# Kernel tuning notes

Hardware: AMD Instinct MI355X
Metric: run time of the kernel (lower is better)

Reference implementation:

```python
import jax, jax.numpy as jnp
import numpy as np

DIM = 768
NUM_HEADS = 12
HEAD_DIM = DIM // NUM_HEADS
H, W = 16, 64
HK, WK = 7, 11
N = H * W
B = 8
SCALE = HEAD_DIM ** -0.5


def build_local_mask():
    # Vectorized version of the original nested loop: for each token (h,w),
    # positions inside the hk x wk window are visible (0), others -inf.
    h_idx = np.repeat(np.arange(H), W)  # [N]
    w_idx = np.tile(np.arange(W), H)    # [N]
    hh = np.arange(H + HK - 1)
    ww = np.arange(W + WK - 1)
    in_h = (hh[None, :] >= h_idx[:, None]) & (hh[None, :] < h_idx[:, None] + HK)  # [N, H+hk-1]
    in_w = (ww[None, :] >= w_idx[:, None]) & (ww[None, :] < w_idx[:, None] + WK)  # [N, W+wk-1]
    visible = in_h[:, :, None] & in_w[:, None, :]  # [N, H+hk-1, W+wk-1]
    mask_big = np.where(visible, 0.0, 1.0).astype(np.float32)
    mask_crop = mask_big[:, HK // 2:H + HK // 2, WK // 2:W + WK // 2].reshape(N, N)
    mask = np.where(mask_crop < 1.0, mask_crop, np.float32(-np.inf))  # [N, N]
    return jnp.asarray(mask)[None, None]  # [1, 1, N, N]


def setup_inputs() -> dict:
    key = jax.random.key(0)
    k1, k2, k3 = jax.random.split(key, 3)
    x = jax.random.normal(k1, (B, N, DIM), dtype=jnp.float32)
    w_qkv = jax.random.normal(k2, (3 * DIM, DIM), dtype=jnp.float32) * 0.02  # torch Linear weight [out,in]
    w_proj = jax.random.normal(k3, (DIM, DIM), dtype=jnp.float32) * 0.02
    b_proj = jnp.zeros((DIM,), dtype=jnp.float32)
    mask = build_local_mask()
    return {"x": x, "w_qkv": w_qkv, "w_proj": w_proj, "b_proj": b_proj, "mask": mask}


def reference(x, w_qkv, w_proj, b_proj, mask):
    Bx, Nx, C = x.shape
    qkv = jnp.einsum('bnc,oc->bno', x, w_qkv)  # [B, N, 3*dim]
    qkv = qkv.reshape(Bx, Nx, 3, NUM_HEADS, HEAD_DIM).transpose(2, 0, 3, 1, 4)  # [3,B,h,N,d]
    q, k, v = qkv[0] * SCALE, qkv[1], qkv[2]
    attn = jnp.einsum('bhnd,bhmd->bhnm', q, k) + mask  # [B,h,N,N] with local -inf mask
    attn = jax.nn.softmax(attn, axis=-1)
    out = jnp.einsum('bhnm,bhmd->bhnd', attn, v)  # [B,h,N,d]
    out = out.transpose(0, 2, 1, 3).reshape(Bx, Nx, C)
    out = jnp.einsum('bnc,oc->bno', out, w_proj) + b_proj
    return out
```

## Files before the change

### kernel.cpp

```cpp
#include <hip/hip_runtime.h>
#include <hip/hip_bf16.h>
#include <stdint.h>

typedef __bf16 bf16;
typedef __bf16 bf16x8 __attribute__((ext_vector_type(8)));
typedef __bf16 bf16x4 __attribute__((ext_vector_type(4)));
typedef float f32x4 __attribute__((ext_vector_type(4)));

#define KDIM 768
#define NHEAD 12
#define HDIM 64
#define NTOK 1024
#define BATCH 8

#define SWZ(row, b) ((b) ^ (((row) & 7) << 4))

__device__ __forceinline__ void gl_lds16(const bf16* g, bf16* l) {
    __builtin_amdgcn_global_load_lds((const __attribute__((address_space(1))) void*)g,
                                     (__attribute__((address_space(3))) void*)l, 16, 0, 0);
}

#define G_MFMA(a, b, c) __builtin_amdgcn_mfma_f32_16x16x32_bf16(a, b, c, 0, 0, 0)
#define VMW(N) asm volatile("s_waitcnt vmcnt(" #N ")" ::: "memory")

__global__ void k_cvt_all(const float* __restrict__ x, const float* __restrict__ wq,
                          const float* __restrict__ wp, bf16* __restrict__ xb,
                          bf16* __restrict__ wqb, bf16* __restrict__ wpb) {
    int b = blockIdx.x;
    const float* src;
    bf16* dst;
    int base;
    if (b < 6144)       { src = x;  dst = xb;  base = b; }
    else if (b < 7872)  { src = wq; dst = wqb; base = b - 6144; }
    else                { src = wp; dst = wpb; base = b - 7872; }
    int i = (base * 256 + threadIdx.x) * 4;
    float4 v = *(const float4*)(src + i);
    bf16x4 o;
    o[0] = (bf16)v.x; o[1] = (bf16)v.y; o[2] = (bf16)v.z; o[3] = (bf16)v.w;
    *(bf16x4*)(dst + i) = o;
}

#define QTILE(S, kA, kB, doA, doB, vmn) do {                                    \
    const char* A8 = (const char*)sA[S];                                        \
    const char* B8 = (const char*)sB[S];                                        \
    bf16x8 af[2], bfr[6];                                                       \
    af[0] = *(const bf16x8*)(A8 + (wr * 64 + 0 + lr) * 64 + kxoff);             \
    af[1] = *(const bf16x8*)(A8 + (wr * 64 + 16 + lr) * 64 + kxoff);            \
    _Pragma("unroll")                                                           \
    for (int n = 0; n < 6; ++n)                                                 \
        bfr[n] = *(const bf16x8*)(B8 + (wc * 96 + n * 16 + lr) * 64 + kxoff);   \
    if (doA) {                                                                  \
        const bf16* p_ = Ast + (size_t)(kA) * 32;                               \
        gl_lds16(p_,                    &sA[(S) ^ 1][t * 8]);                   \
        gl_lds16(p_ + (size_t)64 * KDIM, &sA[(S) ^ 1][t * 8 + 2048]);           \
    }                                                                           \
    __builtin_amdgcn_s_setprio(1);                                              \
    _Pragma("unroll")                                                           \
    for (int m = 0; m < 2; ++m)                                                 \
        _Pragma("unroll")                                                       \
        for (int n = 0; n < 6; ++n)                                             \
            acc[m][n] = G_MFMA(af[m], bfr[n], acc[m][n]);                       \
    __builtin_amdgcn_s_setprio(0);                                              \
    __builtin_amdgcn_s_barrier();                                               \
    af[0] = *(const bf16x8*)(A8 + (wr * 64 + 32 + lr) * 64 + kxoff);            \
    af[1] = *(const bf16x8*)(A8 + (wr * 64 + 48 + lr) * 64 + kxoff);            \
    if (doB) {                                                                  \
        const bf16* p_ = Wst + (size_t)(kB) * 32;                               \
        gl_lds16(p_,                     &sB[S][t * 8]);                        \
        gl_lds16(p_ + (size_t)64 * KDIM,  &sB[S][t * 8 + 2048]);                \
        gl_lds16(p_ + (size_t)128 * KDIM, &sB[S][t * 8 + 4096]);                \
    }                                                                           \
    __builtin_amdgcn_s_setprio(1);                                              \
    _Pragma("unroll")                                                           \
    for (int m = 0; m < 2; ++m)                                                 \
        _Pragma("unroll")                                                       \
        for (int n = 0; n < 6; ++n)                                             \
            acc[m + 2][n] = G_MFMA(af[m], bfr[n], acc[m + 2][n]);               \
    __builtin_amdgcn_s_setprio(0);                                              \
    if ((vmn) == 3) { VMW(3); } else if ((vmn) == 0) { VMW(0); }                \
    __builtin_amdgcn_s_barrier();                                               \
} while (0)

#define GEMM192_PRE(A_PTR, W_PTR)                                               \
    const int t = threadIdx.x;                                                  \
    const int lane = t & 63;                                                    \
    const int wv = t >> 6;                                                      \
    const int wr = wv >> 1, wc = wv & 1;                                        \
    const int lr = lane & 15, lg = lane >> 4;                                   \
    const int kxoff = (lg << 4) ^ (((lr >> 1) & 3) << 4);                       \
    const int srow = t >> 2;                                                    \
    const int spos = ((t & 3) ^ ((t >> 3) & 3)) * 8;                            \
    const int bm = blockIdx.x, bn = blockIdx.y;                                 \
    const bf16* Ab = (A_PTR) + (size_t)bm * 128 * KDIM;                         \
    const bf16* Wb = (W_PTR) + (size_t)bn * 192 * KDIM;                         \
    const bf16* Ast = Ab + (size_t)srow * KDIM + spos;                          \
    const bf16* Wst = Wb + (size_t)srow * KDIM + spos;                          \
    f32x4 acc[4][6] = {};                                                       \
    gl_lds16(Ast,                     &sA[0][t * 8]);                           \
    gl_lds16(Ast + (size_t)64 * KDIM, &sA[0][t * 8 + 2048]);                    \
    gl_lds16(Wst,                      &sB[0][t * 8]);                          \
    gl_lds16(Wst + (size_t)64 * KDIM,  &sB[0][t * 8 + 2048]);                   \
    gl_lds16(Wst + (size_t)128 * KDIM, &sB[0][t * 8 + 4096]);                   \
    gl_lds16(Wst + 32,                      &sB[1][t * 8]);                     \
    gl_lds16(Wst + 32 + (size_t)64 * KDIM,  &sB[1][t * 8 + 2048]);              \
    gl_lds16(Wst + 32 + (size_t)128 * KDIM, &sB[1][t * 8 + 4096]);              \
    VMW(3);                                                                     \
    __builtin_amdgcn_s_barrier();                                               \
    _Pragma("unroll 1")                                                         \
    for (int g = 0; g < 11; ++g) {                                              \
        QTILE(0, 2 * g + 1, 2 * g + 2, 1, 1, 3);                                \
        QTILE(1, 2 * g + 2, 2 * g + 3, 1, 1, 3);                                \
    }                                                                           \
    QTILE(0, 23, 0, 1, 0, 0);                                                   \
    QTILE(1, 0, 0, 0, 0, -1);

__global__ __launch_bounds__(256, 3) void k_gemm_qkv(
    const bf16* __restrict__ A, const bf16* __restrict__ W,
    bf16* __restrict__ qb, bf16* __restrict__ kb, bf16* __restrict__ vb)
{
    __shared__ __attribute__((aligned(16))) bf16 sA[2][4096];
    __shared__ __attribute__((aligned(16))) bf16 sB[2][6144];
    GEMM192_PRE(A, W);

    const float QSC = 0.18033688011112042f;
#pragma unroll
    for (int n = 0; n < 6; ++n) {
        int o = bn * 192 + wc * 96 + n * 16 + lr;
        int s = o / 768;
        int rem = o - s * 768;
        int head = rem >> 6;
        int d = o & 63;
        bf16* dst = (s == 0) ? qb : ((s == 1) ? kb : vb);
        float sc = (s == 0) ? QSC : 1.0f;
#pragma unroll
        for (int m = 0; m < 4; ++m) {
            int grow = bm * 128 + wr * 64 + m * 16 + lg * 4;
            int bidx = grow >> 10;
            int tok = grow & 1023;
            size_t base = (((size_t)bidx * NHEAD + head) * NTOK + tok) * HDIM + d;
#pragma unroll
            for (int r = 0; r < 4; ++r)
                dst[base + (size_t)r * HDIM] = (bf16)(acc[m][n][r] * sc);
        }
    }
}

__global__ __launch_bounds__(256, 3) void k_gemm_proj(
    const bf16* __restrict__ A, const bf16* __restrict__ W,
    const float* __restrict__ bias, float* __restrict__ out)
{
    __shared__ __attribute__((aligned(16))) bf16 sA[2][4096];
    __shared__ __attribute__((aligned(16))) bf16 sB[2][6144];
    GEMM192_PRE(A, W);

#pragma unroll
    for (int n = 0; n < 6; ++n) {
        int col = bn * 192 + wc * 96 + n * 16 + lr;
        float bv = bias[col];
#pragma unroll
        for (int m = 0; m < 4; ++m) {
            int grow = bm * 128 + wr * 64 + m * 16 + lg * 4;
#pragma unroll
            for (int r = 0; r < 4; ++r)
                out[(size_t)(grow + r) * KDIM + col] = acc[m][n][r] + bv;
        }
    }
}

__global__ __launch_bounds__(256) void k_attn(
    const bf16* __restrict__ qbuf, const bf16* __restrict__ kbuf,
    const bf16* __restrict__ vbuf, bf16* __restrict__ ob)
{
    const int x = blockIdx.x;
    const int sub = x >> 3;
    const int bh = (x & 7) * 12 + (sub >> 4);
    const int qblk = sub & 15;
    const int head = bh % NHEAD, bidx = bh / NHEAD;
    const bf16* Q  = qbuf + (size_t)bh * NTOK * HDIM;
    const bf16* Kp = kbuf + (size_t)bh * NTOK * HDIM;
    const bf16* Vp = vbuf + (size_t)bh * NTOK * HDIM;

    const int t = threadIdx.x, lane = t & 63, wv = t >> 6;
    const int lr = lane & 15, lg = lane >> 4, lkb = lg * 8;

    __shared__ bf16 Ks[2][64 * 64];
    __shared__ bf16 vT[2][64 * 64];
    __shared__ bf16 pls[4][16 * 64];

    {
        bf16x8 z = {};
        *(bf16x8*)&pls[wv][lane * 16] = z;
        *(bf16x8*)&pls[wv][lane * 16 + 8] = z;
    }

    bf16x8 qf[2];
#pragma unroll
    for (int ks = 0; ks < 2; ++ks)
        qf[ks] = *(const bf16x8*)(Q + (size_t)(qblk * 64 + wv * 16 + lr) * HDIM + ks * 32 + lkb);

    f32x4 acc[4] = {};
    float lrow[4] = {0.f, 0.f, 0.f, 0.f};

    const int kh0 = (qblk - 3 < 0) ? 0 : qblk - 3;
    const int kh1 = (qblk + 3 > 15) ? 15 : qblk + 3;

    const int sj = t >> 2;
    const int sd = (t & 3) * 16;

    const bf16* ks0 = Kp + (size_t)(kh0 * 64 + sj) * HDIM + sd;
    const bf16* vs0 = Vp + (size_t)(kh0 * 64 + sj) * HDIM + sd;
    bf16x8 gk0 = *(const bf16x8*)ks0, gk1 = *(const bf16x8*)(ks0 + 8);
    bf16x8 gv0 = *(const bf16x8*)vs0, gv1 = *(const bf16x8*)(vs0 + 8);

    char* pb8 = (char*)pls[wv];
    const int wq0 = wv * 16 + lg * 4;
    int cur = 0;

    for (int kh = kh0; kh <= kh1; ++kh) {
        char* kb8 = (char*)Ks[cur];
        char* vb8 = (char*)vT[cur];
        {
            int kbo = sj * 128 + sd * 2;
            *(bf16x8*)(kb8 + SWZ(sj, kbo)) = gk0;
            *(bf16x8*)(kb8 + SWZ(sj, kbo + 16)) = gk1;
        }
#pragma unroll
        for (int ii = 0; ii < 8; ++ii) {
            int d = sd + ii;
            *(bf16*)(vb8 + SWZ(d, (d << 7) + (sj << 1))) = gv0[ii];
        }
#pragma unroll
        for (int ii = 0; ii < 8; ++ii) {
            int d = sd + 8 + ii;
            *(bf16*)(vb8 + SWZ(d, (d << 7) + (sj << 1))) = gv1[ii];
        }
        if (kh < kh1) {
            const bf16* kn = Kp + (size_t)((kh + 1) * 64 + sj) * HDIM + sd;
            const bf16* vn = Vp + (size_t)((kh + 1) * 64 + sj) * HDIM + sd;
            gk0 = *(const bf16x8*)kn; gk1 = *(const bf16x8*)(kn + 8);
            gv0 = *(const bf16x8*)vn; gv1 = *(const bf16x8*)(vn + 8);
        }
        asm volatile("s_waitcnt lgkmcnt(0)" ::: "memory");
        __builtin_amdgcn_s_barrier();

        float psum[4] = {0.f, 0.f, 0.f, 0.f};
#pragma unroll
        for (int jj = 0; jj < 3; ++jj) {
            int j = wv - 1 + jj;
            if (j >= 0 && j <= 3) {
                int key = j * 16 + lr;
                int kbase = key * 128;
                bf16x8 kf0 = *(const bf16x8*)(kb8 + SWZ(key, kbase + lg * 16));
                bf16x8 kf1 = *(const bf16x8*)(kb8 + SWZ(key, kbase + 64 + lg * 16));
                f32x4 sv = {};
                sv = G_MFMA(qf[0], kf0, sv);
                sv = G_MFMA(qf[1], kf1, sv);
#pragma unroll
                for (int r = 0; r < 4; ++r) {
                    int dw = wq0 + r - key;
                    float p = (dw >= -5 && dw <= 5) ? exp2f(sv[r]) : 0.0f;
                    psum[r] += p;
                    int row = lg * 4 + r;
                    *(bf16*)(pb8 + SWZ(row, row * 128 + key * 2)) = (bf16)p;
                }
            }
        }
#pragma unroll
        for (int r = 0; r < 4; ++r) lrow[r] += psum[r];

        bf16x8 pf0 = *(const bf16x8*)(pb8 + SWZ(lr, lr * 128 + lg * 16));
        bf16x8 pf1 = *(const bf16x8*)(pb8 + SWZ(lr, lr * 128 + 64 + lg * 16));
#pragma unroll
        for (int dt = 0; dt < 4; ++dt) {
            int vrow = dt * 16 + lr;
            bf16x8 vf0 = *(const bf16x8*)(vb8 + SWZ(vrow, vrow * 128 + lg * 16));
            bf16x8 vf1 = *(const bf16x8*)(vb8 + SWZ(vrow, vrow * 128 + 64 + lg * 16));
            acc[dt] = G_MFMA(pf0, vf0, acc[dt]);
            acc[dt] = G_MFMA(pf1, vf1, acc[dt]);
        }
        cur ^= 1;
    }

#pragma unroll
    for (int off = 1; off < 16; off <<= 1)
#pragma unroll
        for (int r = 0; r < 4; ++r) lrow[r] += __shfl_xor(lrow[r], off);

#pragma unroll
    for (int r = 0; r < 4; ++r) {
        float inv = 1.0f / lrow[r];
        int tok = qblk * 64 + wv * 16 + lg * 4 + r;
        size_t rowbase = ((size_t)bidx * NTOK + tok) * KDIM + head * HDIM;
#pragma unroll
        for (int dt = 0; dt < 4; ++dt)
            ob[rowbase + dt * 16 + lr] = (bf16)(acc[dt][r] * inv);
    }
}

extern "C" void kernel_launch(void* const* d_in, const int* in_sizes, int n_in,
                              void* d_out, int out_size, void* d_ws, size_t ws_size,
                              hipStream_t stream) {
    const float* x      = (const float*)d_in[0];
    const float* w_qkv  = (const float*)d_in[1];
    const float* w_proj = (const float*)d_in[2];
    const float* b_proj = (const float*)d_in[3];
    float* out = (float*)d_out;

    char* ws = (char*)d_ws;
    bf16* xb  = (bf16*)(ws);
    bf16* wqb = (bf16*)(ws + 12582912);
    bf16* wpb = (bf16*)(ws + 16121856);
    bf16* qb  = (bf16*)(ws + 17301504);
    bf16* kb  = (bf16*)(ws + 29884416);
    bf16* vb  = (bf16*)(ws + 42467328);
    bf16* aob = (bf16*)(ws + 55050240);

    hipLaunchKernelGGL(k_cvt_all, dim3(8448), dim3(256), 0, stream, x, w_qkv, w_proj, xb, wqb, wpb);
    hipLaunchKernelGGL(k_gemm_qkv, dim3(64, 12), dim3(256), 0, stream, xb, wqb, qb, kb, vb);
    hipLaunchKernelGGL(k_attn,     dim3(1536), dim3(256), 0, stream, qb, kb, vb, aob);
    hipLaunchKernelGGL(k_gemm_proj, dim3(64, 4), dim3(256), 0, stream, aob, wpb, b_proj, out);
}
```

Measured before the change: 101.2 us.

## Fuse fp32-to-bf16 conversion of x into the QKV GEMM A-tile loads

The separate pass that converts x to bf16 is removed. The QKV GEMM now streams fp32 x tiles straight into LDS through global_load_lds and converts them to bf16 when it builds the MFMA fragments. This avoids writing and re-reading a 12.5 MB bf16 copy of x. In exchange the A tile takes twice the LDS and load bandwidth per k-step, occupancy drops from 3 to 2 blocks, and every fragment read now costs extra conversion ALU work.

```diff
diff --git a/kernel.cpp b/kernel.cpp
--- a/kernel.cpp
+++ b/kernel.cpp
@@ -19,25 +19,153 @@
     __builtin_amdgcn_global_load_lds((const __attribute__((address_space(1))) void*)g,
                                      (__attribute__((address_space(3))) void*)l, 16, 0, 0);
 }
+__device__ __forceinline__ void gl_lds16f(const float* g, float* l) {
+    __builtin_amdgcn_global_load_lds((const __attribute__((address_space(1))) void*)g,
+                                     (__attribute__((address_space(3))) void*)l, 16, 0, 0);
+}
 
 #define G_MFMA(a, b, c) __builtin_amdgcn_mfma_f32_16x16x32_bf16(a, b, c, 0, 0, 0)
 #define VMW(N) asm volatile("s_waitcnt vmcnt(" #N ")" ::: "memory")
 
-__global__ void k_cvt_all(const float* __restrict__ x, const float* __restrict__ wq,
-                          const float* __restrict__ wp, bf16* __restrict__ xb,
-                          bf16* __restrict__ wqb, bf16* __restrict__ wpb) {
+__global__ void k_cvt_w(const float* __restrict__ wq, const float* __restrict__ wp,
+                        bf16* __restrict__ wqb, bf16* __restrict__ wpb) {
     int b = blockIdx.x;
     const float* src;
     bf16* dst;
     int base;
-    if (b < 6144)       { src = x;  dst = xb;  base = b; }
-    else if (b < 7872)  { src = wq; dst = wqb; base = b - 6144; }
-    else                { src = wp; dst = wpb; base = b - 7872; }
+    if (b < 1728) { src = wq; dst = wqb; base = b; }
+    else          { src = wp; dst = wpb; base = b - 1728; }
     int i = (base * 256 + threadIdx.x) * 4;
     float4 v = *(const float4*)(src + i);
     bf16x4 o;
     o[0] = (bf16)v.x; o[1] = (bf16)v.y; o[2] = (bf16)v.z; o[3] = (bf16)v.w;
     *(bf16x4*)(dst + i) = o;
+}
+
+
+#define AFRAG(dst, A8, row) do {                                                \
+    const int rb_ = (row) * 128;                                                \
+    float4 w0_ = *(const float4*)((A8) + rb_ + a0off);                          \
+    float4 w1_ = *(const float4*)((A8) + rb_ + a1off);                          \
+    dst[0] = (bf16)w0_.x; dst[1] = (bf16)w0_.y;                                 \
+    dst[2] = (bf16)w0_.z; dst[3] = (bf16)w0_.w;                                 \
+    dst[4] = (bf16)w1_.x; dst[5] = (bf16)w1_.y;                                 \
+    dst[6] = (bf16)w1_.z; dst[7] = (bf16)w1_.w;                                 \
+} while (0)
+
+#define QTILEF(S, kA, kB, doA, doB, vmn) do {                                   \
+    const char* A8 = (const char*)sAf[S];                                       \
+    const char* B8 = (const char*)sB[S];                                        \
+    bf16x8 af[2], bfr[6];                                                       \
+    AFRAG(af[0], A8, wr * 64 + 0 + lr);                                         \
+    AFRAG(af[1], A8, wr * 64 + 16 + lr);                                        \
+    _Pragma("unroll")                                                           \
+    for (int n = 0; n < 6; ++n)                                                 \
+        bfr[n] = *(const bf16x8*)(B8 + (wc * 96 + n * 16 + lr) * 64 + kxoff);   \
+    if (doA) {                                                                  \
+        const float* p_ = XAst + (size_t)(kA) * 32;                             \
+        float* d_ = &sAf[(S) ^ 1][t * 4];                                       \
+        gl_lds16f(p_,                       d_);                                \
+        gl_lds16f(p_ + (size_t)32 * KDIM,   d_ + 1024);                         \
+        gl_lds16f(p_ + (size_t)64 * KDIM,   d_ + 2048);                         \
+        gl_lds16f(p_ + (size_t)96 * KDIM,   d_ + 3072);                         \
+    }                                                                           \
+    __builtin_amdgcn_s_setprio(1);                                              \
+    _Pragma("unroll")                                                           \
+    for (int m = 0; m < 2; ++m)                                                 \
+        _Pragma("unroll")                                                       \
+        for (int n = 0; n < 6; ++n)                                             \
+            acc[m][n] = G_MFMA(af[m], bfr[n], acc[m][n]);                       \
+    __builtin_amdgcn_s_setprio(0);                                              \
+    __builtin_amdgcn_s_barrier();                                               \
+    AFRAG(af[0], A8, wr * 64 + 32 + lr);                                        \
+    AFRAG(af[1], A8, wr * 64 + 48 + lr);                                        \
+    if (doB) {                                                                  \
+        const bf16* p_ = Wst + (size_t)(kB) * 32;                               \
+        gl_lds16(p_,                     &sB[S][t * 8]);                        \
+        gl_lds16(p_ + (size_t)64 * KDIM,  &sB[S][t * 8 + 2048]);                \
+        gl_lds16(p_ + (size_t)128 * KDIM, &sB[S][t * 8 + 4096]);                \
+    }                                                                           \
+    __builtin_amdgcn_s_setprio(1);                                              \
+    _Pragma("unroll")                                                           \
+    for (int m = 0; m < 2; ++m)                                                 \
+        _Pragma("unroll")                                                       \
+        for (int n = 0; n < 6; ++n)                                             \
+            acc[m + 2][n] = G_MFMA(af[m], bfr[n], acc[m + 2][n]);               \
+    __builtin_amdgcn_s_setprio(0);                                              \
+    if ((vmn) == 3) { VMW(3); } else if ((vmn) == 0) { VMW(0); }                \
+    __builtin_amdgcn_s_barrier();                                               \
+} while (0)
+
+__global__ __launch_bounds__(256, 2) void k_gemm_qkv(
+    const float* __restrict__ X, const bf16* __restrict__ W,
+    bf16* __restrict__ qb, bf16* __restrict__ kb, bf16* __restrict__ vb)
+{
+    __shared__ __attribute__((aligned(16))) float sAf[2][4096];
+    __shared__ __attribute__((aligned(16))) bf16 sB[2][6144];
+    const int t = threadIdx.x;
+    const int lane = t & 63;
+    const int wv = t >> 6;
+    const int wr = wv >> 1, wc = wv & 1;
+    const int lr = lane & 15, lg = lane >> 4;
+    const int kxoff = (lg << 4) ^ (((lr >> 1) & 3) << 4);
+    const int xorb4 = (lr & 7) << 4;
+    const int a0off = (lg << 5) ^ xorb4;
+    const int a1off = ((lg << 5) | 16) ^ xorb4;
+    const int srow = t >> 2;
+    const int spos = ((t & 3) ^ ((t >> 3) & 3)) * 8;
+    const int bm = blockIdx.x, bn = blockIdx.y;
+    const float* XAst = X + (size_t)(bm * 128 + (t >> 3)) * KDIM
+                          + (size_t)(((t & 7) ^ ((t >> 3) & 7)) * 4);
+    const bf16* Wb = W + (size_t)bn * 192 * KDIM;
+    const bf16* Wst = Wb + (size_t)srow * KDIM + spos;
+    f32x4 acc[4][6] = {};
+
+    {
+        float* d_ = &sAf[0][t * 4];
+        gl_lds16f(XAst,                       d_);
+        gl_lds16f(XAst + (size_t)32 * KDIM,   d_ + 1024);
+        gl_lds16f(XAst + (size_t)64 * KDIM,   d_ + 2048);
+        gl_lds16f(XAst + (size_t)96 * KDIM,   d_ + 3072);
+    }
+    gl_lds16(Wst,                      &sB[0][t * 8]);
+    gl_lds16(Wst + (size_t)64 * KDIM,  &sB[0][t * 8 + 2048]);
+    gl_lds16(Wst + (size_t)128 * KDIM, &sB[0][t * 8 + 4096]);
+    gl_lds16(Wst + 32,                      &sB[1][t * 8]);
+    gl_lds16(Wst + 32 + (size_t)64 * KDIM,  &sB[1][t * 8 + 2048]);
+    gl_lds16(Wst + 32 + (size_t)128 * KDIM, &sB[1][t * 8 + 4096]);
+    VMW(3);
+    __builtin_amdgcn_s_barrier();
+
+#pragma unroll 1
+    for (int g = 0; g < 11; ++g) {
+        QTILEF(0, 2 * g + 1, 2 * g + 2, 1, 1, 3);
+        QTILEF(1, 2 * g + 2, 2 * g + 3, 1, 1, 3);
+    }
+    QTILEF(0, 23, 0, 1, 0, 0);
+    QTILEF(1, 0, 0, 0, 0, -1);
+
+    const float QSC = 0.18033688011112042f;
+#pragma unroll
+    for (int n = 0; n < 6; ++n) {
+        int o = bn * 192 + wc * 96 + n * 16 + lr;
+        int s = o / 768;
+        int rem = o - s * 768;
+        int head = rem >> 6;
+        int d = o & 63;
+        bf16* dst = (s == 0) ? qb : ((s == 1) ? kb : vb);
+        float sc = (s == 0) ? QSC : 1.0f;
+#pragma unroll
+        for (int m = 0; m < 4; ++m) {
+            int grow = bm * 128 + wr * 64 + m * 16 + lg * 4;
+            int bidx = grow >> 10;
+            int tok = grow & 1023;
+            size_t base = (((size_t)bidx * NHEAD + head) * NTOK + tok) * HDIM + d;
+#pragma unroll
+            for (int r = 0; r < 4; ++r)
+                dst[base + (size_t)r * HDIM] = (bf16)(acc[m][n][r] * sc);
+        }
+    }
 }
 
 #define QTILE(S, kA, kB, doA, doB, vmn) do {                                    \
@@ -81,77 +209,43 @@
     __builtin_amdgcn_s_barrier();                                               \
 } while (0)
 
-#define GEMM192_PRE(A_PTR, W_PTR)                                               \
-    const int t = threadIdx.x;                                                  \
-    const int lane = t & 63;                                                    \
-    const int wv = t >> 6;                                                      \
-    const int wr = wv >> 1, wc = wv & 1;                                        \
-    const int lr = lane & 15, lg = lane >> 4;                                   \
-    const int kxoff = (lg << 4) ^ (((lr >> 1) & 3) << 4);                       \
-    const int srow = t >> 2;                                                    \
-    const int spos = ((t & 3) ^ ((t >> 3) & 3)) * 8;                            \
-    const int bm = blockIdx.x, bn = blockIdx.y;                                 \
-    const bf16* Ab = (A_PTR) + (size_t)bm * 128 * KDIM;                         \
-    const bf16* Wb = (W_PTR) + (size_t)bn * 192 * KDIM;                         \
-    const bf16* Ast = Ab + (size_t)srow * KDIM + spos;                          \
-    const bf16* Wst = Wb + (size_t)srow * KDIM + spos;                          \
-    f32x4 acc[4][6] = {};                                                       \
-    gl_lds16(Ast,                     &sA[0][t * 8]);                           \
-    gl_lds16(Ast + (size_t)64 * KDIM, &sA[0][t * 8 + 2048]);                    \
-    gl_lds16(Wst,                      &sB[0][t * 8]);                          \
-    gl_lds16(Wst + (size_t)64 * KDIM,  &sB[0][t * 8 + 2048]);                   \
-    gl_lds16(Wst + (size_t)128 * KDIM, &sB[0][t * 8 + 4096]);                   \
-    gl_lds16(Wst + 32,                      &sB[1][t * 8]);                     \
-    gl_lds16(Wst + 32 + (size_t)64 * KDIM,  &sB[1][t * 8 + 2048]);              \
-    gl_lds16(Wst + 32 + (size_t)128 * KDIM, &sB[1][t * 8 + 4096]);              \
-    VMW(3);                                                                     \
-    __builtin_amdgcn_s_barrier();                                               \
-    _Pragma("unroll 1")                                                         \
-    for (int g = 0; g < 11; ++g) {                                              \
-        QTILE(0, 2 * g + 1, 2 * g + 2, 1, 1, 3);                                \
-        QTILE(1, 2 * g + 2, 2 * g + 3, 1, 1, 3);                                \
-    }                                                                           \
-    QTILE(0, 23, 0, 1, 0, 0);                                                   \
-    QTILE(1, 0, 0, 0, 0, -1);
-
-__global__ __launch_bounds__(256, 3) void k_gemm_qkv(
-    const bf16* __restrict__ A, const bf16* __restrict__ W,
-    bf16* __restrict__ qb, bf16* __restrict__ kb, bf16* __restrict__ vb)
-{
-    __shared__ __attribute__((aligned(16))) bf16 sA[2][4096];
-    __shared__ __attribute__((aligned(16))) bf16 sB[2][6144];
-    GEMM192_PRE(A, W);
-
-    const float QSC = 0.18033688011112042f;
-#pragma unroll
-    for (int n = 0; n < 6; ++n) {
-        int o = bn * 192 + wc * 96 + n * 16 + lr;
-        int s = o / 768;
-        int rem = o - s * 768;
-        int head = rem >> 6;
-        int d = o & 63;
-        bf16* dst = (s == 0) ? qb : ((s == 1) ? kb : vb);
-        float sc = (s == 0) ? QSC : 1.0f;
-#pragma unroll
-        for (int m = 0; m < 4; ++m) {
-            int grow = bm * 128 + wr * 64 + m * 16 + lg * 4;
-            int bidx = grow >> 10;
-            int tok = grow & 1023;
-            size_t base = (((size_t)bidx * NHEAD + head) * NTOK + tok) * HDIM + d;
-#pragma unroll
-            for (int r = 0; r < 4; ++r)
-                dst[base + (size_t)r * HDIM] = (bf16)(acc[m][n][r] * sc);
-        }
-    }
-}
-
 __global__ __launch_bounds__(256, 3) void k_gemm_proj(
     const bf16* __restrict__ A, const bf16* __restrict__ W,
     const float* __restrict__ bias, float* __restrict__ out)
 {
     __shared__ __attribute__((aligned(16))) bf16 sA[2][4096];
     __shared__ __attribute__((aligned(16))) bf16 sB[2][6144];
-    GEMM192_PRE(A, W);
+    const int t = threadIdx.x;
+    const int lane = t & 63;
+    const int wv = t >> 6;
+    const int wr = wv >> 1, wc = wv & 1;
+    const int lr = lane & 15, lg = lane >> 4;
+    const int kxoff = (lg << 4) ^ (((lr >> 1) & 3) << 4);
+    const int srow = t >> 2;
+    const int spos = ((t & 3) ^ ((t >> 3) & 3)) * 8;
+    const int bm = blockIdx.x, bn = blockIdx.y;
+    const bf16* Ab = A + (size_t)bm * 128 * KDIM;
+    const bf16* Wb = W + (size_t)bn * 192 * KDIM;
+    const bf16* Ast = Ab + (size_t)srow * KDIM + spos;
+    const bf16* Wst = Wb + (size_t)srow * KDIM + spos;
+    f32x4 acc[4][6] = {};
+    gl_lds16(Ast,                     &sA[0][t * 8]);
+    gl_lds16(Ast + (size_t)64 * KDIM, &sA[0][t * 8 + 2048]);
+    gl_lds16(Wst,                      &sB[0][t * 8]);
+    gl_lds16(Wst + (size_t)64 * KDIM,  &sB[0][t * 8 + 2048]);
+    gl_lds16(Wst + (size_t)128 * KDIM, &sB[0][t * 8 + 4096]);
+    gl_lds16(Wst + 32,                      &sB[1][t * 8]);
+    gl_lds16(Wst + 32 + (size_t)64 * KDIM,  &sB[1][t * 8 + 2048]);
+    gl_lds16(Wst + 32 + (size_t)128 * KDIM, &sB[1][t * 8 + 4096]);
+    VMW(3);
+    __builtin_amdgcn_s_barrier();
+#pragma unroll 1
+    for (int g = 0; g < 11; ++g) {
+        QTILE(0, 2 * g + 1, 2 * g + 2, 1, 1, 3);
+        QTILE(1, 2 * g + 2, 2 * g + 3, 1, 1, 3);
+    }
+    QTILE(0, 23, 0, 1, 0, 0);
+    QTILE(1, 0, 0, 0, 0, -1);
 
 #pragma unroll
     for (int n = 0; n < 6; ++n) {
@@ -307,16 +401,15 @@
     float* out = (float*)d_out;
 
     char* ws = (char*)d_ws;
-    bf16* xb  = (bf16*)(ws);
-    bf16* wqb = (bf16*)(ws + 12582912);
-    bf16* wpb = (bf16*)(ws + 16121856);
-    bf16* qb  = (bf16*)(ws + 17301504);
-    bf16* kb  = (bf16*)(ws + 29884416);
-    bf16* vb  = (bf16*)(ws + 42467328);
-    bf16* aob = (bf16*)(ws + 55050240);
-
-    hipLaunchKernelGGL(k_cvt_all, dim3(8448), dim3(256), 0, stream, x, w_qkv, w_proj, xb, wqb, wpb);
-    hipLaunchKernelGGL(k_gemm_qkv, dim3(64, 12), dim3(256), 0, stream, xb, wqb, qb, kb, vb);
+    bf16* wqb = (bf16*)(ws);
+    bf16* wpb = (bf16*)(ws + 3538944);
+    bf16* qb  = (bf16*)(ws + 4718592);
+    bf16* kb  = (bf16*)(ws + 17301504);
+    bf16* vb  = (bf16*)(ws + 29884416);
+    bf16* aob = (bf16*)(ws + 42467328);
+
+    hipLaunchKernelGGL(k_cvt_w,    dim3(2304), dim3(256), 0, stream, w_qkv, w_proj, wqb, wpb);
+    hipLaunchKernelGGL(k_gemm_qkv, dim3(64, 12), dim3(256), 0, stream, x, wqb, qb, kb, vb);
     hipLaunchKernelGGL(k_attn,     dim3(1536), dim3(256), 0, stream, qb, kb, vb, aob);
     hipLaunchKernelGGL(k_gemm_proj, dim3(64, 4), dim3(256), 0, stream, aob, wpb, b_proj, out);
 }
```

After: 106.6 us. 1.05x slower.

## Rewrite QKV GEMM with 64-wide K tiles and simple double buffering

Applied to the files above, without the earlier changes.

The QKV projection GEMM moves from 32-wide K steps with a staggered A/B prefetch scheme to 64-wide K tiles (12 iterations). Each tile is fully double-buffered and ends with a full vmcnt(0) wait and one barrier. This halves the number of barriers and loop iterations and issues larger prefetch batches. In exchange, LDS use doubles to 80 KB per block and launch bounds drop from 3 to 2 blocks per CU, which lowers occupancy. The projection GEMM keeps the old scheme, with the macro inlined.

```diff
diff --git a/kernel.cpp b/kernel.cpp
--- a/kernel.cpp
+++ b/kernel.cpp
@@ -40,6 +40,119 @@
     *(bf16x4*)(dst + i) = o;
 }
 
+
+#define TILE64(S, kt) do {                                                      \
+    const char* A8 = (const char*)sA[S];                                        \
+    const char* B8 = (const char*)sB[S];                                        \
+    bf16x8 af[4], bfr[6];                                                       \
+    _Pragma("unroll")                                                           \
+    for (int m = 0; m < 4; ++m)                                                 \
+        af[m] = *(const bf16x8*)(A8 + (wr * 64 + m * 16 + lr) * 128 + k0off);   \
+    _Pragma("unroll")                                                           \
+    for (int n = 0; n < 6; ++n)                                                 \
+        bfr[n] = *(const bf16x8*)(B8 + (wc * 96 + n * 16 + lr) * 128 + k0off);  \
+    if ((kt) < 11) {                                                            \
+        const bf16* p_ = Ast + (size_t)((kt) + 1) * 64;                         \
+        gl_lds16(p_,                      &sA[(S) ^ 1][t * 8]);                 \
+        gl_lds16(p_ + (size_t)32 * KDIM,  &sA[(S) ^ 1][t * 8 + 2048]);          \
+        gl_lds16(p_ + (size_t)64 * KDIM,  &sA[(S) ^ 1][t * 8 + 4096]);          \
+        gl_lds16(p_ + (size_t)96 * KDIM,  &sA[(S) ^ 1][t * 8 + 6144]);          \
+    }                                                                           \
+    __builtin_amdgcn_s_setprio(1);                                              \
+    _Pragma("unroll")                                                           \
+    for (int m = 0; m < 4; ++m)                                                 \
+        _Pragma("unroll")                                                       \
+        for (int n = 0; n < 6; ++n)                                             \
+            acc[m][n] = G_MFMA(af[m], bfr[n], acc[m][n]);                       \
+    __builtin_amdgcn_s_setprio(0);                                              \
+    _Pragma("unroll")                                                           \
+    for (int m = 0; m < 4; ++m)                                                 \
+        af[m] = *(const bf16x8*)(A8 + (wr * 64 + m * 16 + lr) * 128 + k1off);   \
+    _Pragma("unroll")                                                           \
+    for (int n = 0; n < 6; ++n)                                                 \
+        bfr[n] = *(const bf16x8*)(B8 + (wc * 96 + n * 16 + lr) * 128 + k1off);  \
+    if ((kt) < 11) {                                                            \
+        const bf16* p_ = Wst + (size_t)((kt) + 1) * 64;                         \
+        gl_lds16(p_,                       &sB[(S) ^ 1][t * 8]);                \
+        gl_lds16(p_ + (size_t)32 * KDIM,   &sB[(S) ^ 1][t * 8 + 2048]);         \
+        gl_lds16(p_ + (size_t)64 * KDIM,   &sB[(S) ^ 1][t * 8 + 4096]);         \
+        gl_lds16(p_ + (size_t)96 * KDIM,   &sB[(S) ^ 1][t * 8 + 6144]);         \
+        gl_lds16(p_ + (size_t)128 * KDIM,  &sB[(S) ^ 1][t * 8 + 8192]);         \
+        gl_lds16(p_ + (size_t)160 * KDIM,  &sB[(S) ^ 1][t * 8 + 10240]);        \
+    }                                                                           \
+    __builtin_amdgcn_s_setprio(1);                                              \
+    _Pragma("unroll")                                                           \
+    for (int m = 0; m < 4; ++m)                                                 \
+        _Pragma("unroll")                                                       \
+        for (int n = 0; n < 6; ++n)                                             \
+            acc[m][n] = G_MFMA(af[m], bfr[n], acc[m][n]);                       \
+    __builtin_amdgcn_s_setprio(0);                                              \
+    VMW(0);                                                                     \
+    __builtin_amdgcn_s_barrier();                                               \
+} while (0)
+
+__global__ __launch_bounds__(256, 2) void k_gemm_qkv(
+    const bf16* __restrict__ A, const bf16* __restrict__ W,
+    bf16* __restrict__ qb, bf16* __restrict__ kb, bf16* __restrict__ vb)
+{
+    __shared__ __attribute__((aligned(16))) bf16 sA[2][8192];
+    __shared__ __attribute__((aligned(16))) bf16 sB[2][12288];
+    const int t = threadIdx.x;
+    const int lane = t & 63;
+    const int wv = t >> 6;
+    const int wr = wv >> 1, wc = wv & 1;
+    const int lr = lane & 15, lg = lane >> 4;
+    const int xorb = (lr & 7) << 4;
+    const int k0off = (lg << 4) ^ xorb;
+    const int k1off = (64 + (lg << 4)) ^ xorb;
+    const int spos = ((t & 7) ^ ((t >> 3) & 7)) * 8;
+    const int bm = blockIdx.x, bn = blockIdx.y;
+    const bf16* Ast = A + (size_t)(bm * 128 + (t >> 3)) * KDIM + spos;
+    const bf16* Wst = W + (size_t)(bn * 192 + (t >> 3)) * KDIM + spos;
+    f32x4 acc[4][6] = {};
+
+    gl_lds16(Ast,                      &sA[0][t * 8]);
+    gl_lds16(Ast + (size_t)32 * KDIM,  &sA[0][t * 8 + 2048]);
+    gl_lds16(Ast + (size_t)64 * KDIM,  &sA[0][t * 8 + 4096]);
+    gl_lds16(Ast + (size_t)96 * KDIM,  &sA[0][t * 8 + 6144]);
+    gl_lds16(Wst,                       &sB[0][t * 8]);
+    gl_lds16(Wst + (size_t)32 * KDIM,   &sB[0][t * 8 + 2048]);
+    gl_lds16(Wst + (size_t)64 * KDIM,   &sB[0][t * 8 + 4096]);
+    gl_lds16(Wst + (size_t)96 * KDIM,   &sB[0][t * 8 + 6144]);
+    gl_lds16(Wst + (size_t)128 * KDIM,  &sB[0][t * 8 + 8192]);
+    gl_lds16(Wst + (size_t)160 * KDIM,  &sB[0][t * 8 + 10240]);
+    VMW(0);
+    __builtin_amdgcn_s_barrier();
+
+#pragma unroll 1
+    for (int g = 0; g < 6; ++g) {
+        TILE64(0, g * 2);
+        TILE64(1, g * 2 + 1);
+    }
+
+    const float QSC = 0.18033688011112042f;
+#pragma unroll
+    for (int n = 0; n < 6; ++n) {
+        int o = bn * 192 + wc * 96 + n * 16 + lr;
+        int s = o / 768;
+        int rem = o - s * 768;
+        int head = rem >> 6;
+        int d = o & 63;
+        bf16* dst = (s == 0) ? qb : ((s == 1) ? kb : vb);
+        float sc = (s == 0) ? QSC : 1.0f;
+#pragma unroll
+        for (int m = 0; m < 4; ++m) {
+            int grow = bm * 128 + wr * 64 + m * 16 + lg * 4;
+            int bidx = grow >> 10;
+            int tok = grow & 1023;
+            size_t base = (((size_t)bidx * NHEAD + head) * NTOK + tok) * HDIM + d;
+#pragma unroll
+            for (int r = 0; r < 4; ++r)
+                dst[base + (size_t)r * HDIM] = (bf16)(acc[m][n][r] * sc);
+        }
+    }
+}
+
 #define QTILE(S, kA, kB, doA, doB, vmn) do {                                    \
     const char* A8 = (const char*)sA[S];                                        \
     const char* B8 = (const char*)sB[S];                                        \
@@ -81,77 +194,43 @@
     __builtin_amdgcn_s_barrier();                                               \
 } while (0)
 
-#define GEMM192_PRE(A_PTR, W_PTR)                                               \
-    const int t = threadIdx.x;                                                  \
-    const int lane = t & 63;                                                    \
-    const int wv = t >> 6;                                                      \
-    const int wr = wv >> 1, wc = wv & 1;                                        \
-    const int lr = lane & 15, lg = lane >> 4;                                   \
-    const int kxoff = (lg << 4) ^ (((lr >> 1) & 3) << 4);                       \
-    const int srow = t >> 2;                                                    \
-    const int spos = ((t & 3) ^ ((t >> 3) & 3)) * 8;                            \
-    const int bm = blockIdx.x, bn = blockIdx.y;                                 \
-    const bf16* Ab = (A_PTR) + (size_t)bm * 128 * KDIM;                         \
-    const bf16* Wb = (W_PTR) + (size_t)bn * 192 * KDIM;                         \
-    const bf16* Ast = Ab + (size_t)srow * KDIM + spos;                          \
-    const bf16* Wst = Wb + (size_t)srow * KDIM + spos;                          \
-    f32x4 acc[4][6] = {};                                                       \
-    gl_lds16(Ast,                     &sA[0][t * 8]);                           \
-    gl_lds16(Ast + (size_t)64 * KDIM, &sA[0][t * 8 + 2048]);                    \
-    gl_lds16(Wst,                      &sB[0][t * 8]);                          \
-    gl_lds16(Wst + (size_t)64 * KDIM,  &sB[0][t * 8 + 2048]);                   \
-    gl_lds16(Wst + (size_t)128 * KDIM, &sB[0][t * 8 + 4096]);                   \
-    gl_lds16(Wst + 32,                      &sB[1][t * 8]);                     \
-    gl_lds16(Wst + 32 + (size_t)64 * KDIM,  &sB[1][t * 8 + 2048]);              \
-    gl_lds16(Wst + 32 + (size_t)128 * KDIM, &sB[1][t * 8 + 4096]);              \
-    VMW(3);                                                                     \
-    __builtin_amdgcn_s_barrier();                                               \
-    _Pragma("unroll 1")                                                         \
-    for (int g = 0; g < 11; ++g) {                                              \
-        QTILE(0, 2 * g + 1, 2 * g + 2, 1, 1, 3);                                \
-        QTILE(1, 2 * g + 2, 2 * g + 3, 1, 1, 3);                                \
-    }                                                                           \
-    QTILE(0, 23, 0, 1, 0, 0);                                                   \
-    QTILE(1, 0, 0, 0, 0, -1);
-
-__global__ __launch_bounds__(256, 3) void k_gemm_qkv(
-    const bf16* __restrict__ A, const bf16* __restrict__ W,
-    bf16* __restrict__ qb, bf16* __restrict__ kb, bf16* __restrict__ vb)
-{
-    __shared__ __attribute__((aligned(16))) bf16 sA[2][4096];
-    __shared__ __attribute__((aligned(16))) bf16 sB[2][6144];
-    GEMM192_PRE(A, W);
-
-    const float QSC = 0.18033688011112042f;
-#pragma unroll
-    for (int n = 0; n < 6; ++n) {
-        int o = bn * 192 + wc * 96 + n * 16 + lr;
-        int s = o / 768;
-        int rem = o - s * 768;
-        int head = rem >> 6;
-        int d = o & 63;
-        bf16* dst = (s == 0) ? qb : ((s == 1) ? kb : vb);
-        float sc = (s == 0) ? QSC : 1.0f;
-#pragma unroll
-        for (int m = 0; m < 4; ++m) {
-            int grow = bm * 128 + wr * 64 + m * 16 + lg * 4;
-            int bidx = grow >> 10;
-            int tok = grow & 1023;
-            size_t base = (((size_t)bidx * NHEAD + head) * NTOK + tok) * HDIM + d;
-#pragma unroll
-            for (int r = 0; r < 4; ++r)
-                dst[base + (size_t)r * HDIM] = (bf16)(acc[m][n][r] * sc);
-        }
-    }
-}
-
 __global__ __launch_bounds__(256, 3) void k_gemm_proj(
     const bf16* __restrict__ A, const bf16* __restrict__ W,
     const float* __restrict__ bias, float* __restrict__ out)
 {
     __shared__ __attribute__((aligned(16))) bf16 sA[2][4096];
     __shared__ __attribute__((aligned(16))) bf16 sB[2][6144];
-    GEMM192_PRE(A, W);
+    const int t = threadIdx.x;
+    const int lane = t & 63;
+    const int wv = t >> 6;
+    const int wr = wv >> 1, wc = wv & 1;
+    const int lr = lane & 15, lg = lane >> 4;
+    const int kxoff = (lg << 4) ^ (((lr >> 1) & 3) << 4);
+    const int srow = t >> 2;
+    const int spos = ((t & 3) ^ ((t >> 3) & 3)) * 8;
+    const int bm = blockIdx.x, bn = blockIdx.y;
+    const bf16* Ab = A + (size_t)bm * 128 * KDIM;
+    const bf16* Wb = W + (size_t)bn * 192 * KDIM;
+    const bf16* Ast = Ab + (size_t)srow * KDIM + spos;
+    const bf16* Wst = Wb + (size_t)srow * KDIM + spos;
+    f32x4 acc[4][6] = {};
+    gl_lds16(Ast,                     &sA[0][t * 8]);
+    gl_lds16(Ast + (size_t)64 * KDIM, &sA[0][t * 8 + 2048]);
+    gl_lds16(Wst,                      &sB[0][t * 8]);
+    gl_lds16(Wst + (size_t)64 * KDIM,  &sB[0][t * 8 + 2048]);
+    gl_lds16(Wst + (size_t)128 * KDIM, &sB[0][t * 8 + 4096]);
+    gl_lds16(Wst + 32,                      &sB[1][t * 8]);
+    gl_lds16(Wst + 32 + (size_t)64 * KDIM,  &sB[1][t * 8 + 2048]);
+    gl_lds16(Wst + 32 + (size_t)128 * KDIM, &sB[1][t * 8 + 4096]);
+    VMW(3);
+    __builtin_amdgcn_s_barrier();
+#pragma unroll 1
+    for (int g = 0; g < 11; ++g) {
+        QTILE(0, 2 * g + 1, 2 * g + 2, 1, 1, 3);
+        QTILE(1, 2 * g + 2, 2 * g + 3, 1, 1, 3);
+    }
+    QTILE(0, 23, 0, 1, 0, 0);
+    QTILE(1, 0, 0, 0, 0, -1);
 
 #pragma unroll
     for (int n = 0; n < 6; ++n) {
```

After: 97.86 us. 1.03x faster.

## Widen GEMM K-tile to 64 with full double-buffering and one barrier per tile

Applied to the files above, without the earlier changes.

Both GEMM kernels now stage K-tiles of 64 instead of 32. A and B are fully double-buffered and prefetched one tile ahead, the XOR swizzle is widened to 8-way, and each tile ends with a single vmcnt(0) wait and barrier instead of the interleaved half-tile schedule. This cuts barrier and loop overhead per unit of work and simplifies the prefetch pipeline. The cost is twice the LDS per block (80KB), so occupancy drops from 3 to 2 blocks per CU, and the full vmcnt(0) wait each iteration exposes more load latency.

```diff
diff --git a/kernel.cpp b/kernel.cpp
--- a/kernel.cpp
+++ b/kernel.cpp
@@ -40,87 +40,96 @@
     *(bf16x4*)(dst + i) = o;
 }
 
-#define QTILE(S, kA, kB, doA, doB, vmn) do {                                    \
+
+#define TILE64(S, kt) do {                                                      \
     const char* A8 = (const char*)sA[S];                                        \
     const char* B8 = (const char*)sB[S];                                        \
-    bf16x8 af[2], bfr[6];                                                       \
-    af[0] = *(const bf16x8*)(A8 + (wr * 64 + 0 + lr) * 64 + kxoff);             \
-    af[1] = *(const bf16x8*)(A8 + (wr * 64 + 16 + lr) * 64 + kxoff);            \
+    bf16x8 af[4], bfr[6];                                                       \
+    _Pragma("unroll")                                                           \
+    for (int m = 0; m < 4; ++m)                                                 \
+        af[m] = *(const bf16x8*)(A8 + (wr * 64 + m * 16 + lr) * 128 + k0off);   \
     _Pragma("unroll")                                                           \
     for (int n = 0; n < 6; ++n)                                                 \
-        bfr[n] = *(const bf16x8*)(B8 + (wc * 96 + n * 16 + lr) * 64 + kxoff);   \
-    if (doA) {                                                                  \
-        const bf16* p_ = Ast + (size_t)(kA) * 32;                               \
-        gl_lds16(p_,                    &sA[(S) ^ 1][t * 8]);                   \
-        gl_lds16(p_ + (size_t)64 * KDIM, &sA[(S) ^ 1][t * 8 + 2048]);           \
+        bfr[n] = *(const bf16x8*)(B8 + (wc * 96 + n * 16 + lr) * 128 + k0off);  \
+    if ((kt) < 11) {                                                            \
+        const bf16* p_ = Ast + (size_t)((kt) + 1) * 64;                         \
+        gl_lds16(p_,                      &sA[(S) ^ 1][t * 8]);                 \
+        gl_lds16(p_ + (size_t)32 * KDIM,  &sA[(S) ^ 1][t * 8 + 2048]);          \
+        gl_lds16(p_ + (size_t)64 * KDIM,  &sA[(S) ^ 1][t * 8 + 4096]);          \
+        gl_lds16(p_ + (size_t)96 * KDIM,  &sA[(S) ^ 1][t * 8 + 6144]);          \
     }                                                                           \
     __builtin_amdgcn_s_setprio(1);                                              \
     _Pragma("unroll")                                                           \
-    for (int m = 0; m < 2; ++m)                                                 \
+    for (int m = 0; m < 4; ++m)                                                 \
         _Pragma("unroll")                                                       \
         for (int n = 0; n < 6; ++n)                                             \
             acc[m][n] = G_MFMA(af[m], bfr[n], acc[m][n]);                       \
     __builtin_amdgcn_s_setprio(0);                                              \
-    __builtin_amdgcn_s_barrier();                                               \
-    af[0] = *(const bf16x8*)(A8 + (wr * 64 + 32 + lr) * 64 + kxoff);            \
-    af[1] = *(const bf16x8*)(A8 + (wr * 64 + 48 + lr) * 64 + kxoff);            \
-    if (doB) {                                                                  \
-        const bf16* p_ = Wst + (size_t)(kB) * 32;                               \
-        gl_lds16(p_,                     &sB[S][t * 8]);                        \
-        gl_lds16(p_ + (size_t)64 * KDIM,  &sB[S][t * 8 + 2048]);                \
-        gl_lds16(p_ + (size_t)128 * KDIM, &sB[S][t * 8 + 4096]);                \
+    _Pragma("unroll")                                                           \
+    for (int m = 0; m < 4; ++m)                                                 \
+        af[m] = *(const bf16x8*)(A8 + (wr * 64 + m * 16 + lr) * 128 + k1off);   \
+    _Pragma("unroll")                                                           \
+    for (int n = 0; n < 6; ++n)                                                 \
+        bfr[n] = *(const bf16x8*)(B8 + (wc * 96 + n * 16 + lr) * 128 + k1off);  \
+    if ((kt) < 11) {                                                            \
+        const bf16* p_ = Wst + (size_t)((kt) + 1) * 64;                         \
+        gl_lds16(p_,                       &sB[(S) ^ 1][t * 8]);                \
+        gl_lds16(p_ + (size_t)32 * KDIM,   &sB[(S) ^ 1][t * 8 + 2048]);         \
+        gl_lds16(p_ + (size_t)64 * KDIM,   &sB[(S) ^ 1][t * 8 + 4096]);         \
+        gl_lds16(p_ + (size_t)96 * KDIM,   &sB[(S) ^ 1][t * 8 + 6144]);         \
+        gl_lds16(p_ + (size_t)128 * KDIM,  &sB[(S) ^ 1][t * 8 + 8192]);         \
+        gl_lds16(p_ + (size_t)160 * KDIM,  &sB[(S) ^ 1][t * 8 + 10240]);        \
     }                                                                           \
     __builtin_amdgcn_s_setprio(1);                                              \
     _Pragma("unroll")                                                           \
-    for (int m = 0; m < 2; ++m)                                                 \
+    for (int m = 0; m < 4; ++m)                                                 \
         _Pragma("unroll")                                                       \
         for (int n = 0; n < 6; ++n)                                             \
-            acc[m + 2][n] = G_MFMA(af[m], bfr[n], acc[m + 2][n]);               \
+            acc[m][n] = G_MFMA(af[m], bfr[n], acc[m][n]);                       \
     __builtin_amdgcn_s_setprio(0);                                              \
-    if ((vmn) == 3) { VMW(3); } else if ((vmn) == 0) { VMW(0); }                \
+    VMW(0);                                                                     \
     __builtin_amdgcn_s_barrier();                                               \
 } while (0)
 
-#define GEMM192_PRE(A_PTR, W_PTR)                                               \
+#define GEMM64_PRE(A_PTR, W_PTR)                                                \
     const int t = threadIdx.x;                                                  \
     const int lane = t & 63;                                                    \
     const int wv = t >> 6;                                                      \
     const int wr = wv >> 1, wc = wv & 1;                                        \
     const int lr = lane & 15, lg = lane >> 4;                                   \
-    const int kxoff = (lg << 4) ^ (((lr >> 1) & 3) << 4);                       \
-    const int srow = t >> 2;                                                    \
-    const int spos = ((t & 3) ^ ((t >> 3) & 3)) * 8;                            \
+    const int xorb = (lr & 7) << 4;                                             \
+    const int k0off = (lg << 4) ^ xorb;                                         \
+    const int k1off = (64 + (lg << 4)) ^ xorb;                                  \
+    const int spos = ((t & 7) ^ ((t >> 3) & 7)) * 8;                            \
     const int bm = blockIdx.x, bn = blockIdx.y;                                 \
-    const bf16* Ab = (A_PTR) + (size_t)bm * 128 * KDIM;                         \
-    const bf16* Wb = (W_PTR) + (size_t)bn * 192 * KDIM;                         \
-    const bf16* Ast = Ab + (size_t)srow * KDIM + spos;                          \
-    const bf16* Wst = Wb + (size_t)srow * KDIM + spos;                          \
+    const bf16* Ast = (A_PTR) + (size_t)(bm * 128 + (t >> 3)) * KDIM + spos;    \
+    const bf16* Wst = (W_PTR) + (size_t)(bn * 192 + (t >> 3)) * KDIM + spos;    \
     f32x4 acc[4][6] = {};                                                       \
-    gl_lds16(Ast,                     &sA[0][t * 8]);                           \
-    gl_lds16(Ast + (size_t)64 * KDIM, &sA[0][t * 8 + 2048]);                    \
-    gl_lds16(Wst,                      &sB[0][t * 8]);                          \
-    gl_lds16(Wst + (size_t)64 * KDIM,  &sB[0][t * 8 + 2048]);                   \
-    gl_lds16(Wst + (size_t)128 * KDIM, &sB[0][t * 8 + 4096]);                   \
-    gl_lds16(Wst + 32,                      &sB[1][t * 8]);                     \
-    gl_lds16(Wst + 32 + (size_t)64 * KDIM,  &sB[1][t * 8 + 2048]);              \
-    gl_lds16(Wst + 32 + (size_t)128 * KDIM, &sB[1][t * 8 + 4096]);              \
-    VMW(3);                                                                     \
+    gl_lds16(Ast,                      &sA[0][t * 8]);                          \
+    gl_lds16(Ast + (size_t)32 * KDIM,  &sA[0][t * 8 + 2048]);                   \
+    gl_lds16(Ast + (size_t)64 * KDIM,  &sA[0][t * 8 + 4096]);                   \
+    gl_lds16(Ast + (size_t)96 * KDIM,  &sA[0][t * 8 + 6144]);                   \
+    gl_lds16(Wst,                       &sB[0][t * 8]);                         \
+    gl_lds16(Wst + (size_t)32 * KDIM,   &sB[0][t * 8 + 2048]);                  \
+    gl_lds16(Wst + (size_t)64 * KDIM,   &sB[0][t * 8 + 4096]);                  \
+    gl_lds16(Wst + (size_t)96 * KDIM,   &sB[0][t * 8 + 6144]);                  \
+    gl_lds16(Wst + (size_t)128 * KDIM,  &sB[0][t * 8 + 8192]);                  \
+    gl_lds16(Wst + (size_t)160 * KDIM,  &sB[0][t * 8 + 10240]);                 \
+    VMW(0);                                                                     \
     __builtin_amdgcn_s_barrier();                                               \
     _Pragma("unroll 1")                                                         \
-    for (int g = 0; g < 11; ++g) {                                              \
-        QTILE(0, 2 * g + 1, 2 * g + 2, 1, 1, 3);                                \
-        QTILE(1, 2 * g + 2, 2 * g + 3, 1, 1, 3);                                \
-    }                                                                           \
-    QTILE(0, 23, 0, 1, 0, 0);                                                   \
-    QTILE(1, 0, 0, 0, 0, -1);
-
-__global__ __launch_bounds__(256, 3) void k_gemm_qkv(
+    for (int g = 0; g < 6; ++g) {                                               \
+        TILE64(0, g * 2);                                                       \
+        TILE64(1, g * 2 + 1);                                                   \
+    }
+
+__global__ __launch_bounds__(256, 2) void k_gemm_qkv(
     const bf16* __restrict__ A, const bf16* __restrict__ W,
     bf16* __restrict__ qb, bf16* __restrict__ kb, bf16* __restrict__ vb)
 {
-    __shared__ __attribute__((aligned(16))) bf16 sA[2][4096];
-    __shared__ __attribute__((aligned(16))) bf16 sB[2][6144];
-    GEMM192_PRE(A, W);
+    __shared__ __attribute__((aligned(16))) bf16 sA[2][8192];
+    __shared__ __attribute__((aligned(16))) bf16 sB[2][12288];
+    GEMM64_PRE(A, W);
 
     const float QSC = 0.18033688011112042f;
 #pragma unroll
@@ -145,13 +154,13 @@
     }
 }
 
-__global__ __launch_bounds__(256, 3) void k_gemm_proj(
+__global__ __launch_bounds__(256, 2) void k_gemm_proj(
     const bf16* __restrict__ A, const bf16* __restrict__ W,
     const float* __restrict__ bias, float* __restrict__ out)
 {
-    __shared__ __attribute__((aligned(16))) bf16 sA[2][4096];
-    __shared__ __attribute__((aligned(16))) bf16 sB[2][6144];
-    GEMM192_PRE(A, W);
+    __shared__ __attribute__((aligned(16))) bf16 sA[2][8192];
+    __shared__ __attribute__((aligned(16))) bf16 sB[2][12288];
+    GEMM64_PRE(A, W);
 
 #pragma unroll
     for (int n = 0; n < 6; ++n) {
```

New measurement: 91.20 us, median of 3. -9.9%, faster.
